# Performance work log

Hardware: AMD Instinct MI355X
Metric: run time of the kernel (lower is better)

## Reference

```python
import jax, jax.numpy as jnp
import numpy as np

N_NODES = 100000
N_EDGES = 3200000
IN_CH = 128
HID_CH = 128
OUT_CH = 64
N_GRAPHS = 128


def gcn_conv(x, edge_index, edge_weight, W, b):
    # x: [N, F_in]; edge_index: [2, E] (row=source j, col=target i); edge_weight: [E]
    N = x.shape[0]
    x = x @ W  # [N, F_out]
    # add self-loops with weight 1 (PyG GCNConv default, fill_value=1.0)
    loop = jnp.arange(N, dtype=edge_index.dtype)
    row = jnp.concatenate([edge_index[0], loop])
    col = jnp.concatenate([edge_index[1], loop])
    w = jnp.concatenate([edge_weight, jnp.ones((N,), dtype=x.dtype)])
    # symmetric normalization: deg computed at target (col)
    deg = jax.ops.segment_sum(w, col, num_segments=N)
    dinv = jnp.where(deg > 0, jax.lax.rsqrt(deg), 0.0)
    norm = dinv[row] * w * dinv[col]  # [E+N]
    msg = x[row] * norm[:, None]  # gather + scale
    out = jax.ops.segment_sum(msg, col, num_segments=N)  # scatter-add
    return out + b


def setup_inputs() -> dict:
    key = jax.random.key(0)
    ks = jax.random.split(key, 10)
    x = jax.random.normal(ks[0], (N_NODES, IN_CH), dtype=jnp.float32)
    edge_index = jax.random.randint(ks[1], (2, N_EDGES), 0, N_NODES, dtype=jnp.int64)
    edge_attr = jax.random.uniform(ks[2], (N_EDGES,), dtype=jnp.float32)
    batch = jnp.sort(jax.random.randint(ks[3], (N_NODES,), 0, N_GRAPHS, dtype=jnp.int64))
    # GCNConv weights (glorot) and zero bias, classifier xavier_normal + bias 0.1
    def glorot(k, fi, fo):
        s = jnp.sqrt(6.0 / (fi + fo))
        return jax.random.uniform(k, (fi, fo), minval=-s, maxval=s, dtype=jnp.float32)
    W1 = glorot(ks[4], IN_CH, HID_CH)
    b1 = jnp.zeros((HID_CH,), dtype=jnp.float32)
    W2 = glorot(ks[5], HID_CH, HID_CH)
    b2 = jnp.zeros((HID_CH,), dtype=jnp.float32)
    std = jnp.sqrt(2.0 / (HID_CH + OUT_CH))
    Wc = jax.random.normal(ks[6], (HID_CH, OUT_CH), dtype=jnp.float32) * std
    bc = jnp.full((OUT_CH,), 0.1, dtype=jnp.float32)
    return {"x": x, "edge_index": edge_index, "edge_attr": edge_attr,
            "batch": batch, "W1": W1, "b1": b1, "W2": W2, "b2": b2,
            "Wc": Wc, "bc": bc}


def reference(x, edge_index, edge_attr, batch, W1, b1, W2, b2, Wc, bc):
    h = jax.nn.relu(gcn_conv(x, edge_index, edge_attr, W1, b1))
    h = jax.nn.relu(gcn_conv(h, edge_index, edge_attr, W2, b2))
    pooled = jax.ops.segment_sum(h, batch, num_segments=N_GRAPHS)  # [G, HID]
    logits = pooled @ Wc + bc
    return jax.nn.sigmoid(logits)
```

## Files before the change

kernel.cpp:

```cpp
#include <hip/hip_runtime.h>
#include <hip/hip_bf16.h>
#include <hip/hip_fp16.h>


#define FEAT 128
#define OUTC 64
#define PAD  80
#define NB_SHIFT 8
#define BINSZ 256
#define CAP 9216
#define TILE_A 4096
#define LDW 136

typedef _Float16 half8 __attribute__((ext_vector_type(8)));
typedef float    f32x4 __attribute__((ext_vector_type(4)));

__global__ __launch_bounds__(256) void bin_edges(const int* __restrict__ ei,
                                                 const float* __restrict__ ew,
                                                 int* __restrict__ binCnt,
                                                 int2* __restrict__ binned,
                                                 int E, int nbins) {
    __shared__ int hist[512];
    __shared__ int base[512];
    int tid = threadIdx.x;
    int e0 = blockIdx.x * TILE_A;
    for (int i = tid; i < nbins; i += 256) hist[i] = 0;
    __syncthreads();
    for (int i = 0; i < TILE_A; i += 256) {
        int e = e0 + i + tid;
        if (e < E) atomicAdd(&hist[ei[E + e] >> NB_SHIFT], 1);
    }
    __syncthreads();
    for (int i = tid; i < nbins; i += 256) {
        int h = hist[i];
        base[i] = (h > 0) ? atomicAdd(&binCnt[i], h) : 0;
        hist[i] = 0;
    }
    __syncthreads();
    for (int i = 0; i < TILE_A; i += 256) {
        int e = e0 + i + tid;
        if (e < E) {
            int col = ei[E + e];
            int row = ei[e];
            float w = ew[e];
            int b  = col >> NB_SHIFT;
            int lp = atomicAdd(&hist[b], 1);
            int pos = base[b] + lp;
            if (pos < CAP) {
                int cl = col & (BINSZ - 1);
                binned[(size_t)b * CAP + pos] = make_int2((cl << 24) | row, __float_as_int(w));
            }
        }
    }
}

__global__ __launch_bounds__(256) void bin_scatter(const int2* __restrict__ binned,
                                                   const int* __restrict__ binCnt,
                                                   int* __restrict__ cnt,
                                                   int2* __restrict__ buf,
                                                   float* __restrict__ dinv, int N) {
    __shared__ int   lcnt[BINSZ];
    __shared__ float dsum[BINSZ];
    int tid = threadIdx.x;
    int b = blockIdx.x;
    lcnt[tid] = 0;
    dsum[tid] = 0.f;
    __syncthreads();
    int node0 = b << NB_SHIFT;
    int ne = min(binCnt[b], CAP);
    const int2* src = binned + (size_t)b * CAP;
    for (int i = tid; i < ne; i += 256) {
        int2 m = src[i];
        int cl  = ((unsigned)m.x) >> 24;
        int row = m.x & 0xFFFFFF;
        int pos = atomicAdd(&lcnt[cl], 1);
        if (pos < PAD) buf[(size_t)(node0 + cl) * PAD + pos] = make_int2(row, m.y);
        atomicAdd(&dsum[cl], __int_as_float(m.y));
    }
    __syncthreads();
    int node = node0 + tid;
    if (node < N) {
        cnt[node]  = min(lcnt[tid], PAD);
        dinv[node] = rsqrtf(1.0f + dsum[tid]);
    }
}

__global__ __launch_bounds__(256) void gemm_mfma(const float* __restrict__ X,
                                                 const float* __restrict__ W,
                                                 const float* __restrict__ dinv,
                                                 __half* __restrict__ Y, int N) {
    __shared__ _Float16 Wt[128 * LDW];
    __shared__ float ldsDinv[128];
    int tid = threadIdx.x;
    int row0 = blockIdx.x * 128;
    for (int i = tid; i < FEAT * FEAT; i += 256) {
        int k = i >> 7, n = i & 127;
        Wt[n * LDW + k] = (_Float16)W[i];
    }
    if (tid < 128) ldsDinv[tid] = dinv[min(row0 + tid, N - 1)];
    __syncthreads();

    int wave = tid >> 6;
    int lane = tid & 63;
    int m    = lane & 15;
    int quad = lane >> 4;

    f32x4 acc[2][8];
    #pragma unroll
    for (int rt = 0; rt < 2; ++rt)
        #pragma unroll
        for (int ct = 0; ct < 8; ++ct)
            acc[rt][ct] = (f32x4){0.f, 0.f, 0.f, 0.f};

    int rowA[2];
    rowA[0] = min(row0 + (wave * 2 + 0) * 16 + m, N - 1);
    rowA[1] = min(row0 + (wave * 2 + 1) * 16 + m, N - 1);

    #pragma unroll
    for (int kt = 0; kt < 4; ++kt) {
        int k0 = kt * 32;
        half8 a[2];
        #pragma unroll
        for (int rt = 0; rt < 2; ++rt) {
            const float4* p = (const float4*)(X + (size_t)rowA[rt] * FEAT + k0 + quad * 8);
            float4 f0 = p[0], f1 = p[1];
            half8 h;
            h[0] = (_Float16)f0.x; h[1] = (_Float16)f0.y;
            h[2] = (_Float16)f0.z; h[3] = (_Float16)f0.w;
            h[4] = (_Float16)f1.x; h[5] = (_Float16)f1.y;
            h[6] = (_Float16)f1.z; h[7] = (_Float16)f1.w;
            a[rt] = h;
        }
        #pragma unroll
        for (int ct = 0; ct < 8; ++ct) {
            half8 b = *(const half8*)&Wt[(ct * 16 + m) * LDW + k0 + quad * 8];
            acc[0][ct] = __builtin_amdgcn_mfma_f32_16x16x32_f16(a[0], b, acc[0][ct], 0, 0, 0);
            acc[1][ct] = __builtin_amdgcn_mfma_f32_16x16x32_f16(a[1], b, acc[1][ct], 0, 0, 0);
        }
    }

    #pragma unroll
    for (int rt = 0; rt < 2; ++rt) {
        int lr0 = (wave * 2 + rt) * 16 + quad * 4;
        #pragma unroll
        for (int r = 0; r < 4; ++r) {
            int gr = row0 + lr0 + r;
            if (gr < N) {
                float d = ldsDinv[lr0 + r];
                #pragma unroll
                for (int ct = 0; ct < 8; ++ct)
                    Y[(size_t)gr * FEAT + ct * 16 + m] = __float2half(d * acc[rt][ct][r]);
            }
        }
    }
}

__global__ __launch_bounds__(256) void agg_kernel(const __half* __restrict__ Y,
                                                  const int2* __restrict__ buf,
                                                  const int* __restrict__ cnt,
                                                  const float* __restrict__ dinv,
                                                  const float* __restrict__ bias,
                                                  float* __restrict__ Out, int N) {
    int node = blockIdx.x * 4 + (threadIdx.x >> 6);
    int lane = threadIdx.x & 63;
    if (node >= N) return;
    int c = cnt[node];
    const int2* meta = buf + (size_t)node * PAD;
    float2 a0 = __half22float2(((const __half2*)(Y + (size_t)node * FEAT))[lane]);
    float2 a1 = {0.f, 0.f}, a2 = {0.f, 0.f}, a3 = {0.f, 0.f};
    int t = 0;
    for (; t + 8 <= c; t += 8) {
        int2 m0 = meta[t],     m1 = meta[t + 1], m2 = meta[t + 2], m3 = meta[t + 3];
        int2 m4 = meta[t + 4], m5 = meta[t + 5], m6 = meta[t + 6], m7 = meta[t + 7];
        float2 v0 = __half22float2(((const __half2*)(Y + (size_t)m0.x * FEAT))[lane]);
        float2 v1 = __half22float2(((const __half2*)(Y + (size_t)m1.x * FEAT))[lane]);
        float2 v2 = __half22float2(((const __half2*)(Y + (size_t)m2.x * FEAT))[lane]);
        float2 v3 = __half22float2(((const __half2*)(Y + (size_t)m3.x * FEAT))[lane]);
        float2 v4 = __half22float2(((const __half2*)(Y + (size_t)m4.x * FEAT))[lane]);
        float2 v5 = __half22float2(((const __half2*)(Y + (size_t)m5.x * FEAT))[lane]);
        float2 v6 = __half22float2(((const __half2*)(Y + (size_t)m6.x * FEAT))[lane]);
        float2 v7 = __half22float2(((const __half2*)(Y + (size_t)m7.x * FEAT))[lane]);
        float w0 = __int_as_float(m0.y), w1 = __int_as_float(m1.y);
        float w2 = __int_as_float(m2.y), w3 = __int_as_float(m3.y);
        float w4 = __int_as_float(m4.y), w5 = __int_as_float(m5.y);
        float w6 = __int_as_float(m6.y), w7 = __int_as_float(m7.y);
        a0.x += w0 * v0.x; a0.y += w0 * v0.y;
        a1.x += w1 * v1.x; a1.y += w1 * v1.y;
        a2.x += w2 * v2.x; a2.y += w2 * v2.y;
        a3.x += w3 * v3.x; a3.y += w3 * v3.y;
        a0.x += w4 * v4.x; a0.y += w4 * v4.y;
        a1.x += w5 * v5.x; a1.y += w5 * v5.y;
        a2.x += w6 * v6.x; a2.y += w6 * v6.y;
        a3.x += w7 * v7.x; a3.y += w7 * v7.y;
    }
    for (; t < c; ++t) {
        int2 m = meta[t];
        float w = __int_as_float(m.y);
        float2 v = __half22float2(((const __half2*)(Y + (size_t)m.x * FEAT))[lane]);
        a0.x += w * v.x;
        a0.y += w * v.y;
    }
    float accx = (a0.x + a1.x) + (a2.x + a3.x);
    float accy = (a0.y + a1.y) + (a2.y + a3.y);
    float d = dinv[node];
    int cc = lane * 2;
    float2 b = *(const float2*)(bias + cc);
    float2 o = {fmaxf(d * accx + b.x, 0.f), fmaxf(d * accy + b.y, 0.f)};
    *(float2*)(Out + (size_t)node * FEAT + cc) = o;
}

__global__ void pool_kernel(const float* __restrict__ H, const int* __restrict__ batch,
                            float* __restrict__ pooled, int N, int chunk) {
    int f  = threadIdx.x;
    int n0 = blockIdx.x * chunk;
    if (n0 >= N) return;
    int n1 = min(n0 + chunk, N);
    float acc = 0.f;
    int cur = batch[n0];
    for (int n = n0; n < n1; ++n) {
        int g = batch[n];
        if (g != cur) {
            atomicAdd(&pooled[cur * FEAT + f], acc);
            acc = 0.f;
            cur = g;
        }
        acc += H[(size_t)n * FEAT + f];
    }
    atomicAdd(&pooled[cur * FEAT + f], acc);
}

__global__ void classify_kernel(const float* __restrict__ pooled, const float* __restrict__ Wc,
                                const float* __restrict__ bc, float* __restrict__ out) {
    int g = blockIdx.x;
    int c = threadIdx.x;
    float acc = bc[c];
    const float* pr = pooled + g * FEAT;
    for (int k = 0; k < FEAT; ++k) acc += pr[k] * Wc[k * OUTC + c];
    out[g * OUTC + c] = 1.0f / (1.0f + expf(-acc));
}

extern "C" void kernel_launch(void* const* d_in, const int* in_sizes, int n_in,
                              void* d_out, int out_size, void* d_ws, size_t ws_size,
                              hipStream_t stream) {
    const float* x     = (const float*)d_in[0];
    const int*   ei    = (const int*)d_in[1];
    const float* ew    = (const float*)d_in[2];
    const int*   batch = (const int*)d_in[3];
    const float* W1    = (const float*)d_in[4];
    const float* b1    = (const float*)d_in[5];
    const float* W2    = (const float*)d_in[6];
    const float* b2    = (const float*)d_in[7];
    const float* Wc    = (const float*)d_in[8];
    const float* bc    = (const float*)d_in[9];
    float* out = (float*)d_out;

    const int N = in_sizes[0] / FEAT;
    const int E = in_sizes[2];
    const int G = out_size / OUTC;
    const int nbins = (N + BINSZ - 1) / BINSZ;

    char* w = (char*)d_ws;
    size_t off = 0;
    auto alloc = [&](size_t bytes) {
        void* p = w + off;
        off = (off + bytes + 255) & ~(size_t)255;
        return p;
    };
    float*  dinv   = (float*)alloc((size_t)N * 4);
    int*    cnt    = (int*)alloc((size_t)N * 4);
    int*    binCnt = (int*)alloc((size_t)nbins * 4);
    int2*   binned = (int2*)alloc((size_t)nbins * CAP * 8);
    int2*   buf    = (int2*)alloc((size_t)N * PAD * 8);
    __half* bufY   = (__half*)alloc((size_t)N * FEAT * 2);
    float*  bufH   = (float*)alloc((size_t)N * FEAT * 4);
    float*  pooled = (float*)alloc((size_t)G * FEAT * 4);
    (void)ws_size;

    hipMemsetAsync(binCnt, 0, (size_t)nbins * 4, stream);
    hipMemsetAsync(pooled, 0, (size_t)G * FEAT * 4, stream);

    bin_edges<<<(E + TILE_A - 1) / TILE_A, 256, 0, stream>>>(ei, ew, binCnt, binned, E, nbins);
    bin_scatter<<<nbins, 256, 0, stream>>>(binned, binCnt, cnt, buf, dinv, N);

    const int gemm_blocks = (N + 127) / 128;
    const int agg_blocks  = (N + 3) / 4;

    gemm_mfma<<<gemm_blocks, 256, 0, stream>>>(x, W1, dinv, bufY, N);
    agg_kernel<<<agg_blocks, 256, 0, stream>>>(bufY, buf, cnt, dinv, b1, bufH, N);
    gemm_mfma<<<gemm_blocks, 256, 0, stream>>>(bufH, W2, dinv, bufY, N);
    agg_kernel<<<agg_blocks, 256, 0, stream>>>(bufY, buf, cnt, dinv, b2, bufH, N);

    const int chunk = 256;
    pool_kernel<<<(N + chunk - 1) / chunk, FEAT, 0, stream>>>(bufH, batch, pooled, N, chunk);
    classify_kernel<<<G, OUTC, 0, stream>>>(pooled, Wc, bc, out);
}
```

Measured before the change: 583.3 us.

## Pre-transpose weights once and accumulate aggregation in packed half2 FMA

Adds a small kernel that converts and transposes each weight matrix to fp16 once. The GEMM then reads B fragments straight from global/L2 instead of rebuilding an LDS copy and syncing in every block, and reads dinv directly. Edge weights are stored as duplicated fp16 pairs so aggregation can use packed __hfma2 into eight half2 accumulators, which are summed in fp32 at the end. This cuts per-edge conversion and FMA instructions but risks precision loss from fp16 accumulation over up to 80 neighbours.

```diff
diff --git a/kernel.cpp b/kernel.cpp
--- a/kernel.cpp
+++ b/kernel.cpp
@@ -10,7 +10,6 @@
 #define BINSZ 256
 #define CAP 9216
 #define TILE_A 4096
-#define LDW 136
 
 typedef _Float16 half8 __attribute__((ext_vector_type(8)));
 typedef float    f32x4 __attribute__((ext_vector_type(4)));
@@ -73,9 +72,12 @@
         int2 m = src[i];
         int cl  = ((unsigned)m.x) >> 24;
         int row = m.x & 0xFFFFFF;
+        float wf = __int_as_float(m.y);
         int pos = atomicAdd(&lcnt[cl], 1);
-        if (pos < PAD) buf[(size_t)(node0 + cl) * PAD + pos] = make_int2(row, m.y);
-        atomicAdd(&dsum[cl], __int_as_float(m.y));
+        unsigned short hs = __half_as_ushort(__float2half(wf));
+        int wpk = (int)hs | ((int)hs << 16);
+        if (pos < PAD) buf[(size_t)(node0 + cl) * PAD + pos] = make_int2(row, wpk);
+        atomicAdd(&dsum[cl], wf);
     }
     __syncthreads();
     int node = node0 + tid;
@@ -85,21 +87,18 @@
     }
 }
 
+__global__ void wt_prep(const float* __restrict__ W, _Float16* __restrict__ Wt) {
+    int i = blockIdx.x * 256 + threadIdx.x;
+    int n = i >> 7, k = i & 127;
+    Wt[(size_t)n * FEAT + k] = (_Float16)W[(size_t)k * FEAT + n];
+}
+
 __global__ __launch_bounds__(256) void gemm_mfma(const float* __restrict__ X,
-                                                 const float* __restrict__ W,
+                                                 const _Float16* __restrict__ Wt,
                                                  const float* __restrict__ dinv,
                                                  __half* __restrict__ Y, int N) {
-    __shared__ _Float16 Wt[128 * LDW];
-    __shared__ float ldsDinv[128];
-    int tid = threadIdx.x;
+    int tid  = threadIdx.x;
     int row0 = blockIdx.x * 128;
-    for (int i = tid; i < FEAT * FEAT; i += 256) {
-        int k = i >> 7, n = i & 127;
-        Wt[n * LDW + k] = (_Float16)W[i];
-    }
-    if (tid < 128) ldsDinv[tid] = dinv[min(row0 + tid, N - 1)];
-    __syncthreads();
-
     int wave = tid >> 6;
     int lane = tid & 63;
     int m    = lane & 15;
@@ -113,8 +112,8 @@
             acc[rt][ct] = (f32x4){0.f, 0.f, 0.f, 0.f};
 
     int rowA[2];
-    rowA[0] = min(row0 + (wave * 2 + 0) * 16 + m, N - 1);
-    rowA[1] = min(row0 + (wave * 2 + 1) * 16 + m, N - 1);
+    rowA[0] = min(row0 + wave * 32 + m, N - 1);
+    rowA[1] = min(row0 + wave * 32 + 16 + m, N - 1);
 
     #pragma unroll
     for (int kt = 0; kt < 4; ++kt) {
@@ -133,7 +132,7 @@
         }
         #pragma unroll
         for (int ct = 0; ct < 8; ++ct) {
-            half8 b = *(const half8*)&Wt[(ct * 16 + m) * LDW + k0 + quad * 8];
+            half8 b = *(const half8*)&Wt[(size_t)(ct * 16 + m) * FEAT + k0 + quad * 8];
             acc[0][ct] = __builtin_amdgcn_mfma_f32_16x16x32_f16(a[0], b, acc[0][ct], 0, 0, 0);
             acc[1][ct] = __builtin_amdgcn_mfma_f32_16x16x32_f16(a[1], b, acc[1][ct], 0, 0, 0);
         }
@@ -141,12 +140,12 @@
 
     #pragma unroll
     for (int rt = 0; rt < 2; ++rt) {
-        int lr0 = (wave * 2 + rt) * 16 + quad * 4;
+        int lr0 = wave * 32 + rt * 16 + quad * 4;
         #pragma unroll
         for (int r = 0; r < 4; ++r) {
             int gr = row0 + lr0 + r;
             if (gr < N) {
-                float d = ldsDinv[lr0 + r];
+                float d = dinv[gr];
                 #pragma unroll
                 for (int ct = 0; ct < 8; ++ct)
                     Y[(size_t)gr * FEAT + ct * 16 + m] = __float2half(d * acc[rt][ct][r]);
@@ -166,42 +165,41 @@
     if (node >= N) return;
     int c = cnt[node];
     const int2* meta = buf + (size_t)node * PAD;
-    float2 a0 = __half22float2(((const __half2*)(Y + (size_t)node * FEAT))[lane]);
-    float2 a1 = {0.f, 0.f}, a2 = {0.f, 0.f}, a3 = {0.f, 0.f};
+    float2 self = __half22float2(((const __half2*)(Y + (size_t)node * FEAT))[lane]);
+    __half2 z = __floats2half2_rn(0.f, 0.f);
+    __half2 h0 = z, h1 = z, h2 = z, h3 = z, h4 = z, h5 = z, h6 = z, h7 = z;
     int t = 0;
     for (; t + 8 <= c; t += 8) {
         int2 m0 = meta[t],     m1 = meta[t + 1], m2 = meta[t + 2], m3 = meta[t + 3];
         int2 m4 = meta[t + 4], m5 = meta[t + 5], m6 = meta[t + 6], m7 = meta[t + 7];
-        float2 v0 = __half22float2(((const __half2*)(Y + (size_t)m0.x * FEAT))[lane]);
-        float2 v1 = __half22float2(((const __half2*)(Y + (size_t)m1.x * FEAT))[lane]);
-        float2 v2 = __half22float2(((const __half2*)(Y + (size_t)m2.x * FEAT))[lane]);
-        float2 v3 = __half22float2(((const __half2*)(Y + (size_t)m3.x * FEAT))[lane]);
-        float2 v4 = __half22float2(((const __half2*)(Y + (size_t)m4.x * FEAT))[lane]);
-        float2 v5 = __half22float2(((const __half2*)(Y + (size_t)m5.x * FEAT))[lane]);
-        float2 v6 = __half22float2(((const __half2*)(Y + (size_t)m6.x * FEAT))[lane]);
-        float2 v7 = __half22float2(((const __half2*)(Y + (size_t)m7.x * FEAT))[lane]);
-        float w0 = __int_as_float(m0.y), w1 = __int_as_float(m1.y);
-        float w2 = __int_as_float(m2.y), w3 = __int_as_float(m3.y);
-        float w4 = __int_as_float(m4.y), w5 = __int_as_float(m5.y);
-        float w6 = __int_as_float(m6.y), w7 = __int_as_float(m7.y);
-        a0.x += w0 * v0.x; a0.y += w0 * v0.y;
-        a1.x += w1 * v1.x; a1.y += w1 * v1.y;
-        a2.x += w2 * v2.x; a2.y += w2 * v2.y;
-        a3.x += w3 * v3.x; a3.y += w3 * v3.y;
-        a0.x += w4 * v4.x; a0.y += w4 * v4.y;
-        a1.x += w5 * v5.x; a1.y += w5 * v5.y;
-        a2.x += w6 * v6.x; a2.y += w6 * v6.y;
-        a3.x += w7 * v7.x; a3.y += w7 * v7.y;
+        __half2 v0 = ((const __half2*)(Y + (size_t)m0.x * FEAT))[lane];
+        __half2 v1 = ((const __half2*)(Y + (size_t)m1.x * FEAT))[lane];
+        __half2 v2 = ((const __half2*)(Y + (size_t)m2.x * FEAT))[lane];
+        __half2 v3 = ((const __half2*)(Y + (size_t)m3.x * FEAT))[lane];
+        __half2 v4 = ((const __half2*)(Y + (size_t)m4.x * FEAT))[lane];
+        __half2 v5 = ((const __half2*)(Y + (size_t)m5.x * FEAT))[lane];
+        __half2 v6 = ((const __half2*)(Y + (size_t)m6.x * FEAT))[lane];
+        __half2 v7 = ((const __half2*)(Y + (size_t)m7.x * FEAT))[lane];
+        h0 = __hfma2(*(const __half2*)&m0.y, v0, h0);
+        h1 = __hfma2(*(const __half2*)&m1.y, v1, h1);
+        h2 = __hfma2(*(const __half2*)&m2.y, v2, h2);
+        h3 = __hfma2(*(const __half2*)&m3.y, v3, h3);
+        h4 = __hfma2(*(const __half2*)&m4.y, v4, h4);
+        h5 = __hfma2(*(const __half2*)&m5.y, v5, h5);
+        h6 = __hfma2(*(const __half2*)&m6.y, v6, h6);
+        h7 = __hfma2(*(const __half2*)&m7.y, v7, h7);
     }
     for (; t < c; ++t) {
         int2 m = meta[t];
-        float w = __int_as_float(m.y);
-        float2 v = __half22float2(((const __half2*)(Y + (size_t)m.x * FEAT))[lane]);
-        a0.x += w * v.x;
-        a0.y += w * v.y;
-    }
-    float accx = (a0.x + a1.x) + (a2.x + a3.x);
-    float accy = (a0.y + a1.y) + (a2.y + a3.y);
+        __half2 v = ((const __half2*)(Y + (size_t)m.x * FEAT))[lane];
+        h0 = __hfma2(*(const __half2*)&m.y, v, h0);
+    }
+    float2 f0 = __half22float2(h0), f1 = __half22float2(h1);
+    float2 f2 = __half22float2(h2), f3 = __half22float2(h3);
+    float2 f4 = __half22float2(h4), f5 = __half22float2(h5);
+    float2 f6 = __half22float2(h6), f7 = __half22float2(h7);
+    float accx = self.x + ((f0.x + f1.x) + (f2.x + f3.x)) + ((f4.x + f5.x) + (f6.x + f7.x));
+    float accy = self.y + ((f0.y + f1.y) + (f2.y + f3.y)) + ((f4.y + f5.y) + (f6.y + f7.y));
     float d = dinv[node];
     int cc = lane * 2;
     float2 b = *(const float2*)(bias + cc);
@@ -266,14 +264,16 @@
         off = (off + bytes + 255) & ~(size_t)255;
         return p;
     };
-    float*  dinv   = (float*)alloc((size_t)N * 4);
-    int*    cnt    = (int*)alloc((size_t)N * 4);
-    int*    binCnt = (int*)alloc((size_t)nbins * 4);
-    int2*   binned = (int2*)alloc((size_t)nbins * CAP * 8);
-    int2*   buf    = (int2*)alloc((size_t)N * PAD * 8);
-    __half* bufY   = (__half*)alloc((size_t)N * FEAT * 2);
-    float*  bufH   = (float*)alloc((size_t)N * FEAT * 4);
-    float*  pooled = (float*)alloc((size_t)G * FEAT * 4);
+    float*     dinv   = (float*)alloc((size_t)N * 4);
+    int*       cnt    = (int*)alloc((size_t)N * 4);
+    int*       binCnt = (int*)alloc((size_t)nbins * 4);
+    int2*      binned = (int2*)alloc((size_t)nbins * CAP * 8);
+    int2*      buf    = (int2*)alloc((size_t)N * PAD * 8);
+    __half*    bufY   = (__half*)alloc((size_t)N * FEAT * 2);
+    float*     bufH   = (float*)alloc((size_t)N * FEAT * 4);
+    float*     pooled = (float*)alloc((size_t)G * FEAT * 4);
+    _Float16*  wt1    = (_Float16*)alloc((size_t)FEAT * FEAT * 2);
+    _Float16*  wt2    = (_Float16*)alloc((size_t)FEAT * FEAT * 2);
     (void)ws_size;
 
     hipMemsetAsync(binCnt, 0, (size_t)nbins * 4, stream);
@@ -281,13 +281,15 @@
 
     bin_edges<<<(E + TILE_A - 1) / TILE_A, 256, 0, stream>>>(ei, ew, binCnt, binned, E, nbins);
     bin_scatter<<<nbins, 256, 0, stream>>>(binned, binCnt, cnt, buf, dinv, N);
+    wt_prep<<<64, 256, 0, stream>>>(W1, wt1);
+    wt_prep<<<64, 256, 0, stream>>>(W2, wt2);
 
     const int gemm_blocks = (N + 127) / 128;
     const int agg_blocks  = (N + 3) / 4;
 
-    gemm_mfma<<<gemm_blocks, 256, 0, stream>>>(x, W1, dinv, bufY, N);
+    gemm_mfma<<<gemm_blocks, 256, 0, stream>>>(x, wt1, dinv, bufY, N);
     agg_kernel<<<agg_blocks, 256, 0, stream>>>(bufY, buf, cnt, dinv, b1, bufH, N);
-    gemm_mfma<<<gemm_blocks, 256, 0, stream>>>(bufH, W2, dinv, bufY, N);
+    gemm_mfma<<<gemm_blocks, 256, 0, stream>>>(bufH, wt2, dinv, bufY, N);
     agg_kernel<<<agg_blocks, 256, 0, stream>>>(bufY, buf, cnt, dinv, b2, bufH, N);
 
     const int chunk = 256;
```

Measured after the change: 598.9 us. +2.7%, slower.
